# Kernel optimization log

Hardware: AMD Instinct MI355X
Metric: run time of the kernel (lower is better)

Reference implementation:

```python
import jax, jax.numpy as jnp
import numpy as np

N, IN_DIM, HID, OUT_DIM = 1024, 128, 128, 128


def setup_inputs() -> dict:
    key = jax.random.key(0)
    ks = jax.random.split(key, 7)
    s_in = 1.0 / np.sqrt(IN_DIM)
    s_h = 1.0 / np.sqrt(HID)
    return {
        "x": jax.random.normal(ks[0], (N, IN_DIM), jnp.float32),
        "W1": jax.random.normal(ks[1], (IN_DIM, HID), jnp.float32) * s_in,
        "b1": jax.random.normal(ks[2], (HID,), jnp.float32) * s_in,
        "W2": jax.random.normal(ks[3], (HID, 1), jnp.float32) * s_h,
        "b2": jax.random.normal(ks[4], (1,), jnp.float32) * s_h,
        "Wg": jax.random.normal(ks[5], (IN_DIM, OUT_DIM), jnp.float32) * s_in,
        "bg": jax.random.normal(ks[6], (OUT_DIM,), jnp.float32) * s_in,
    }


def reference(x, W1, b1, W2, b2, Wg, bg):
    # Pairwise abs-diff: [N, N, in_dim]
    diff = jnp.abs(x[:, None, :] - x[None, :, :])
    # 2-layer MLP -> scalar edge logit, then sigmoid -> dense adjacency [N, N]
    h = jax.nn.relu(jnp.einsum("ijd,dh->ijh", diff, W1) + b1)
    adj = jax.nn.sigmoid(jnp.einsum("ijh,ho->ijo", h, W2)[..., 0] + b2[0])
    # sigmoid > 0 everywhere => dense_to_sparse keeps ALL N^2 edges incl. diagonal;
    # PyG gcn_norm then adds no extra self-loops. Symmetric GCN normalization:
    deg = adj.sum(axis=1)  # adj is symmetric (|x_i - x_j| symmetric)
    dinv = jax.lax.rsqrt(deg)
    a_norm = dinv[:, None] * adj * dinv[None, :]
    out = a_norm @ (x @ Wg) + bg
    out = jnp.where(out > 0, out, 0.2 * out)  # leaky_relu(0.2)
    return out, adj
```

## Files before the change

kernel.cpp:

```cpp
#include <hip/hip_runtime.h>
#include <hip/hip_bf16.h>
#include <math.h>

typedef __attribute__((ext_vector_type(8))) _Float16 half8;
typedef __attribute__((ext_vector_type(2))) _Float16 half2v;
typedef __attribute__((ext_vector_type(4))) float f32x4;
typedef __attribute__((ext_vector_type(4))) unsigned int u32x4;

#define NPT 1024
#define D   128

__device__ __forceinline__ unsigned int absdiff_pk(unsigned int a, unsigned int b) {
  half2v d = __builtin_bit_cast(half2v, a) - __builtin_bit_cast(half2v, b);
  return __builtin_bit_cast(unsigned int, d) & 0x7FFF7FFFu;
}
__device__ __forceinline__ unsigned int pk_max(unsigned int a, unsigned int b) {
  unsigned int r;
  asm("v_pk_max_f16 %0, %1, %2" : "=v"(r) : "v"(a), "v"(b));
  return r;
}
__device__ __forceinline__ unsigned int pkrtz(float lo, float hi) {
  return __builtin_bit_cast(unsigned int, __builtin_amdgcn_cvt_pkrtz(lo, hi));
}
__device__ __forceinline__ float fdot2(unsigned int a, unsigned int b, float c) {
  return __builtin_amdgcn_fdot2(__builtin_bit_cast(half2v, a),
                                __builtin_bit_cast(half2v, b), c, false);
}

__global__ __launch_bounds__(128) void k_prep(const float* __restrict__ x,
                                              const float* __restrict__ W1,
                                              const float* __restrict__ Wg,
                                              float* __restrict__ deg,
                                              unsigned short* __restrict__ xsw,
                                              unsigned short* __restrict__ w1p,
                                              unsigned short* __restrict__ xwghT) {
  __shared__ float xi[D];
  const int i = blockIdx.x;
  const int t = threadIdx.x;
  const float xv = x[i * D + t];
  xi[t] = xv;
  if (t == 0) deg[i] = 0.f;
  const _Float16 hv = (_Float16)xv;
  const int byte = i * 256 + ((2 * t) ^ ((i & 7) << 4));
  *(unsigned short*)((unsigned char*)xsw + byte) =
      __builtin_bit_cast(unsigned short, hv);
  if (i < 128) {
    const _Float16 wv = (_Float16)W1[t * 128 + i];
    w1p[((t >> 3) * 128 + i) * 8 + (t & 7)] = __builtin_bit_cast(unsigned short, wv);
  }
  __syncthreads();
  float a0 = 0.f, a1 = 0.f, a2 = 0.f, a3 = 0.f;
#pragma unroll 8
  for (int k = 0; k < D; k += 4) {
    a0 += xi[k + 0] * Wg[(k + 0) * D + t];
    a1 += xi[k + 1] * Wg[(k + 1) * D + t];
    a2 += xi[k + 2] * Wg[(k + 2) * D + t];
    a3 += xi[k + 3] * Wg[(k + 3) * D + t];
  }
  const _Float16 av = (_Float16)((a0 + a1) + (a2 + a3));
  xwghT[t * NPT + i] = __builtin_bit_cast(unsigned short, av);
}

__global__ __launch_bounds__(256, 2) void k_adj(const unsigned short* __restrict__ xsw,
                                                const unsigned short* __restrict__ w1p,
                                                const float* __restrict__ b1,
                                                const float* __restrict__ W2,
                                                const float* __restrict__ b2,
                                                float* __restrict__ adj) {
  __shared__ float sbuf[4][17 * 68];
  const int tid  = threadIdx.x;
  const int lane = tid & 63;
  const int w    = tid >> 6;
  const int l15  = lane & 15;
  const int g    = lane >> 4;
  const int i   = blockIdx.x * 4 + w;
  const int c   = blockIdx.y;
  const int i2  = 1023 - i;
  const int a   = i >> 4;
  const int n_i = 64 - a;
  const int ustart = c * 16;
  const int uend   = (c == 3) ? 65 : (ustart + 16);
  const int len    = uend - ustart;
  const int nvals  = len * 16;
  const int asc    = (blockIdx.y >> 1) & 1;

  half8 w1f[4][8];
#pragma unroll
  for (int ks = 0; ks < 4; ++ks)
#pragma unroll
    for (int ht = 0; ht < 8; ++ht)
      w1f[ks][ht] = *(const half8*)(w1p + ((ks * 4 + g) * 128 + ht * 16 + l15) * 8);

  unsigned int nb1pk[8][2], w2pk[8][2];
  float c0 = 0.f;
#pragma unroll
  for (int ht = 0; ht < 8; ++ht) {
    const f32x4 bv = *(const f32x4*)&b1[ht * 16 + g * 4];
    const f32x4 wv = *(const f32x4*)&W2[ht * 16 + g * 4];
    c0 += bv[0] * wv[0] + bv[1] * wv[1] + bv[2] * wv[2] + bv[3] * wv[3];
    nb1pk[ht][0] = pkrtz(-bv[0], -bv[1]);
    nb1pk[ht][1] = pkrtz(-bv[2], -bv[3]);
    w2pk[ht][0] = pkrtz(wv[0], wv[1]);
    w2pk[ht][1] = pkrtz(wv[2], wv[3]);
  }
  c0 += __shfl_xor(c0, 16);
  c0 += __shfl_xor(c0, 32);
  const float B2 = b2[0] + c0;

  const unsigned char* xsb = (const unsigned char*)xsw;
  const unsigned char* jlane = xsb + l15 * 256;
  const int sxJ = (l15 & 7) << 4;
  const int kb0 = (0 * 64 + g * 16) ^ sxJ;
  const int kb1 = (1 * 64 + g * 16) ^ sxJ;
  const int kb2 = (2 * 64 + g * 16) ^ sxJ;
  const int kb3 = (3 * 64 + g * 16) ^ sxJ;

  float* sbw = sbuf[w];
  u32x4 xiu[4];
  int row_cur = -1;

  u32x4 jr0, jr1, jr2, jr3;
  {
    const int u0 = asc ? ustart : (uend - 1);
    const int grp0 = (u0 < n_i) ? (a + u0) : (u0 - 1);
    const unsigned char* cur = jlane + grp0 * 4096;
    jr0 = *(const u32x4*)(cur + kb0);
    jr1 = *(const u32x4*)(cur + kb1);
    jr2 = *(const u32x4*)(cur + kb2);
    jr3 = *(const u32x4*)(cur + kb3);
  }

#pragma unroll 1
  for (int t = 0; t < len; ++t) {
    const int u = asc ? (ustart + t) : (uend - 1 - t);
    const int row = (u < n_i) ? i : i2;
    if (row != row_cur) {
      row_cur = row;
      const unsigned char* xrow = xsb + row * 256;
      const int sxI = (row & 7) << 4;
#pragma unroll
      for (int ks = 0; ks < 4; ++ks)
        xiu[ks] = *(const u32x4*)(xrow + ((ks * 64 + g * 16) ^ sxI));
    }
    const int tn = (t + 1 < len) ? (t + 1) : t;
    const int un = asc ? (ustart + tn) : (uend - 1 - tn);
    const int grpn = (un < n_i) ? (a + un) : (un - 1);
    const unsigned char* nrow = jlane + grpn * 4096;

    f32x4 acc[8];
#pragma unroll
    for (int ht = 0; ht < 8; ++ht) acc[ht] = f32x4{0.f, 0.f, 0.f, 0.f};

    __builtin_amdgcn_s_setprio(1);
    {
      u32x4 afu;
#pragma unroll
      for (int p4 = 0; p4 < 4; ++p4) afu[p4] = absdiff_pk(jr0[p4], xiu[0][p4]);
      jr0 = *(const u32x4*)(nrow + kb0);
      const half8 af = __builtin_bit_cast(half8, afu);
#pragma unroll
      for (int ht = 0; ht < 8; ++ht)
        acc[ht] = __builtin_amdgcn_mfma_f32_16x16x32_f16(w1f[0][ht], af, acc[ht], 0, 0, 0);
    }
    {
      u32x4 afu;
#pragma unroll
      for (int p4 = 0; p4 < 4; ++p4) afu[p4] = absdiff_pk(jr1[p4], xiu[1][p4]);
      jr1 = *(const u32x4*)(nrow + kb1);
      const half8 af = __builtin_bit_cast(half8, afu);
#pragma unroll
      for (int ht = 0; ht < 8; ++ht)
        acc[ht] = __builtin_amdgcn_mfma_f32_16x16x32_f16(w1f[1][ht], af, acc[ht], 0, 0, 0);
    }
    {
      u32x4 afu;
#pragma unroll
      for (int p4 = 0; p4 < 4; ++p4) afu[p4] = absdiff_pk(jr2[p4], xiu[2][p4]);
      jr2 = *(const u32x4*)(nrow + kb2);
      const half8 af = __builtin_bit_cast(half8, afu);
#pragma unroll
      for (int ht = 0; ht < 8; ++ht)
        acc[ht] = __builtin_amdgcn_mfma_f32_16x16x32_f16(w1f[2][ht], af, acc[ht], 0, 0, 0);
    }
    {
      u32x4 afu;
#pragma unroll
      for (int p4 = 0; p4 < 4; ++p4) afu[p4] = absdiff_pk(jr3[p4], xiu[3][p4]);
      jr3 = *(const u32x4*)(nrow + kb3);
      const half8 af = __builtin_bit_cast(half8, afu);
#pragma unroll
      for (int ht = 0; ht < 8; ++ht)
        acc[ht] = __builtin_amdgcn_mfma_f32_16x16x32_f16(w1f[3][ht], af, acc[ht], 0, 0, 0);
    }
    __builtin_amdgcn_s_setprio(0);

    float sA = 0.f, sB = 0.f, sC = 0.f, sD = 0.f;
#pragma unroll
    for (int ht = 0; ht < 8; ht += 2) {
      unsigned int h0a = pk_max(pkrtz(acc[ht][0], acc[ht][1]), nb1pk[ht][0]);
      unsigned int h0b = pk_max(pkrtz(acc[ht][2], acc[ht][3]), nb1pk[ht][1]);
      unsigned int h1a = pk_max(pkrtz(acc[ht + 1][0], acc[ht + 1][1]), nb1pk[ht + 1][0]);
      unsigned int h1b = pk_max(pkrtz(acc[ht + 1][2], acc[ht + 1][3]), nb1pk[ht + 1][1]);
      sA = fdot2(h0a, w2pk[ht][0], sA);
      sB = fdot2(h0b, w2pk[ht][1], sB);
      sC = fdot2(h1a, w2pk[ht + 1][0], sC);
      sD = fdot2(h1b, w2pk[ht + 1][1], sD);
    }
    sbw[t * 68 + lane] = (sA + sB) + (sC + sD);
  }

#pragma unroll 1
  for (int it = 0; it < 5; ++it) {
    const int p = it * 64 + lane;
    if (p < nvals) {
      const int tt = p >> 4;
      const int j = p & 15;
      const int u = asc ? (ustart + tt) : (uend - 1 - tt);
      const int row = (u < n_i) ? i : i2;
      const int grp = (u < n_i) ? (a + u) : (u - 1);
      const float s = sbw[tt * 68 + j] + sbw[tt * 68 + 16 + j] +
                      sbw[tt * 68 + 32 + j] + sbw[tt * 68 + 48 + j];
      const float sig = 1.f / (1.f + __expf(-(s + B2)));
      adj[row * NPT + grp * 16 + j] = sig;
    }
  }
}

__global__ __launch_bounds__(256) void k_symdeg(float* __restrict__ adj,
                                                float* __restrict__ deg) {
  __shared__ float lds[4][16][17];
  const int tid  = threadIdx.x;
  const int lane = tid & 63;
  const int w    = tid >> 6;
  const int r16 = lane & 15;
  const int c4  = (lane >> 4) * 4;

  if (blockIdx.x < 504) {
    const int t = blockIdx.x * 4 + w;
    int R = (int)((1.0f + sqrtf(1.0f + 8.0f * (float)t)) * 0.5f);
    if (R * (R - 1) / 2 > t) --R;
    if ((R + 1) * R / 2 <= t) ++R;
    const int C = t - R * (R - 1) / 2;

    const f32x4 v = *(const f32x4*)&adj[(C * 16 + r16) * NPT + R * 16 + c4];
    float rs = (v[0] + v[1]) + (v[2] + v[3]);
    rs += __shfl_xor(rs, 16);
    rs += __shfl_xor(rs, 32);
    if (lane < 16) atomicAdd(&deg[C * 16 + r16], rs);
#pragma unroll
    for (int e = 0; e < 4; ++e) lds[w][c4 + e][r16] = v[e];
    f32x4 o;
#pragma unroll
    for (int e = 0; e < 4; ++e) o[e] = lds[w][r16][c4 + e];
    *(f32x4*)&adj[(R * 16 + r16) * NPT + C * 16 + c4] = o;
    float cs = (o[0] + o[1]) + (o[2] + o[3]);
    cs += __shfl_xor(cs, 16);
    cs += __shfl_xor(cs, 32);
    if (lane < 16) atomicAdd(&deg[R * 16 + r16], cs);
  } else {
    const int T = (blockIdx.x - 504) * 4 + w;
    const f32x4 v = *(const f32x4*)&adj[(T * 16 + r16) * NPT + T * 16 + c4];
    float rs = (v[0] + v[1]) + (v[2] + v[3]);
    rs += __shfl_xor(rs, 16);
    rs += __shfl_xor(rs, 32);
    if (lane < 16) atomicAdd(&deg[T * 16 + r16], rs);
  }
}

__global__ __launch_bounds__(128) void k_d1(const float* __restrict__ adj,
                                            const unsigned short* __restrict__ xwghT,
                                            const float* __restrict__ deg,
                                            const float* __restrict__ bg,
                                            float* __restrict__ outp) {
  __shared__ unsigned short dvh[NPT];
  const int tid  = threadIdx.x;
  const int lane = tid & 63;
  const int w    = tid >> 6;
  const int l15  = lane & 15;
  const int g    = lane >> 4;
  const int i0 = blockIdx.x * 16;
  const int t0 = (blockIdx.y * 2 + w) * 16;

#pragma unroll
  for (int it = 0; it < 8; ++it) {
    const int idx = it * 128 + tid;
    const _Float16 dh = (_Float16)rsqrtf(deg[idx]);
    dvh[idx] = __builtin_bit_cast(unsigned short, dh);
  }
  __syncthreads();

  f32x4 acc{0.f, 0.f, 0.f, 0.f};
#pragma unroll 2
  for (int ch = 0; ch < 32; ++ch) {
    const int kofs = ch * 32 + g * 8;
    const half8 af = *(const half8*)(xwghT + (t0 + l15) * NPT + kofs);
    const f32x4 av0 = *(const f32x4*)&adj[(i0 + l15) * NPT + kofs];
    const f32x4 av1 = *(const f32x4*)&adj[(i0 + l15) * NPT + kofs + 4];
    const half2v* dq = (const half2v*)(dvh + kofs);
    u32x4 bu;
    bu[0] = __builtin_bit_cast(unsigned int,
        half2v(__builtin_bit_cast(half2v, pkrtz(av0[0], av0[1])) * dq[0]));
    bu[1] = __builtin_bit_cast(unsigned int,
        half2v(__builtin_bit_cast(half2v, pkrtz(av0[2], av0[3])) * dq[1]));
    bu[2] = __builtin_bit_cast(unsigned int,
        half2v(__builtin_bit_cast(half2v, pkrtz(av1[0], av1[1])) * dq[2]));
    bu[3] = __builtin_bit_cast(unsigned int,
        half2v(__builtin_bit_cast(half2v, pkrtz(av1[2], av1[3])) * dq[3]));
    acc = __builtin_amdgcn_mfma_f32_16x16x32_f16(__builtin_bit_cast(half8, af),
                                                 __builtin_bit_cast(half8, bu), acc, 0, 0, 0);
  }
  const float di = rsqrtf(deg[i0 + l15]);
  const f32x4 bgv = *(const f32x4*)&bg[t0 + g * 4];
  f32x4 o;
#pragma unroll
  for (int r = 0; r < 4; ++r) {
    const float v = acc[r] * di + bgv[r];
    o[r] = v > 0.f ? v : 0.2f * v;
  }
  *(f32x4*)&outp[(i0 + l15) * D + t0 + g * 4] = o;
}

extern "C" void kernel_launch(void* const* d_in, const int* in_sizes, int n_in,
                              void* d_out, int out_size, void* d_ws, size_t ws_size,
                              hipStream_t stream) {
  const float* x  = (const float*)d_in[0];
  const float* W1 = (const float*)d_in[1];
  const float* b1 = (const float*)d_in[2];
  const float* W2 = (const float*)d_in[3];
  const float* b2 = (const float*)d_in[4];
  const float* Wg = (const float*)d_in[5];
  const float* bg = (const float*)d_in[6];

  float* outp = (float*)d_out;
  float* adj  = outp + NPT * D;
  unsigned char* ws = (unsigned char*)d_ws;
  float* deg            = (float*)ws;
  unsigned short* xsw   = (unsigned short*)(ws + 4096);
  unsigned short* w1p   = (unsigned short*)(ws + 4096 + 262144);
  unsigned short* xwghT = (unsigned short*)(ws + 4096 + 262144 + 32768);

  k_prep<<<NPT, 128, 0, stream>>>(x, W1, Wg, deg, xsw, w1p, xwghT);
  k_adj<<<dim3(128, 4), 256, 0, stream>>>(xsw, w1p, b1, W2, b2, adj);
  k_symdeg<<<520, 256, 0, stream>>>(adj, deg);
  k_d1<<<dim3(64, 4), 128, 0, stream>>>(adj, xwghT, deg, bg, outp);
}
```

Baseline: 44.08 us.

## Split hidden dimension across wave pairs in k_adj and widen k_d1 blocks

k_adj now assigns each row to a pair of waves that each compute half of the 128 hidden units, halving per-wave W1 fragment registers and accumulators. This raises occupancy (launch bounds 3) and doubles the grid, at the cost of an added block barrier and an LDS reduction over eight partials. k_d1 now processes all 128 output columns per block using 4 waves with two MFMA tiles each. The adj tile and degree scaling are then converted once per block rather than four times across blocks, though the grid shrinks to 64 blocks.

New measurement: 53.62 us. +21.6%, slower.

```diff
diff --git a/kernel.cpp b/kernel.cpp
--- a/kernel.cpp
+++ b/kernel.cpp
@@ -61,19 +61,21 @@
   xwghT[t * NPT + i] = __builtin_bit_cast(unsigned short, av);
 }
 
-__global__ __launch_bounds__(256, 2) void k_adj(const unsigned short* __restrict__ xsw,
+__global__ __launch_bounds__(256, 3) void k_adj(const unsigned short* __restrict__ xsw,
                                                 const unsigned short* __restrict__ w1p,
                                                 const float* __restrict__ b1,
                                                 const float* __restrict__ W2,
                                                 const float* __restrict__ b2,
                                                 float* __restrict__ adj) {
-  __shared__ float sbuf[4][17 * 68];
+  __shared__ float sbuf[2][17 * 136];
   const int tid  = threadIdx.x;
   const int lane = tid & 63;
   const int w    = tid >> 6;
   const int l15  = lane & 15;
   const int g    = lane >> 4;
-  const int i   = blockIdx.x * 4 + w;
+  const int hh   = w & 1;
+  const int pair = w >> 1;
+  const int i   = blockIdx.x * 2 + pair;
   const int c   = blockIdx.y;
   const int i2  = 1023 - i;
   const int a   = i >> 4;
@@ -82,26 +84,32 @@
   const int uend   = (c == 3) ? 65 : (ustart + 16);
   const int len    = uend - ustart;
   const int nvals  = len * 16;
-  const int asc    = (blockIdx.y >> 1) & 1;
-
-  half8 w1f[4][8];
+  const int asc    = (blockIdx.x ^ (blockIdx.y >> 1)) & 1;
+
+  half8 w1f[4][4];
 #pragma unroll
   for (int ks = 0; ks < 4; ++ks)
 #pragma unroll
-    for (int ht = 0; ht < 8; ++ht)
-      w1f[ks][ht] = *(const half8*)(w1p + ((ks * 4 + g) * 128 + ht * 16 + l15) * 8);
-
-  unsigned int nb1pk[8][2], w2pk[8][2];
+    for (int ht2 = 0; ht2 < 4; ++ht2)
+      w1f[ks][ht2] = *(const half8*)(w1p +
+          ((ks * 4 + g) * 128 + hh * 64 + ht2 * 16 + l15) * 8);
+
+  unsigned int nb1pk[4][2], w2pk[4][2];
   float c0 = 0.f;
 #pragma unroll
   for (int ht = 0; ht < 8; ++ht) {
     const f32x4 bv = *(const f32x4*)&b1[ht * 16 + g * 4];
     const f32x4 wv = *(const f32x4*)&W2[ht * 16 + g * 4];
     c0 += bv[0] * wv[0] + bv[1] * wv[1] + bv[2] * wv[2] + bv[3] * wv[3];
-    nb1pk[ht][0] = pkrtz(-bv[0], -bv[1]);
-    nb1pk[ht][1] = pkrtz(-bv[2], -bv[3]);
-    w2pk[ht][0] = pkrtz(wv[0], wv[1]);
-    w2pk[ht][1] = pkrtz(wv[2], wv[3]);
+  }
+#pragma unroll
+  for (int ht2 = 0; ht2 < 4; ++ht2) {
+    const f32x4 bv = *(const f32x4*)&b1[hh * 64 + ht2 * 16 + g * 4];
+    const f32x4 wv = *(const f32x4*)&W2[hh * 64 + ht2 * 16 + g * 4];
+    nb1pk[ht2][0] = pkrtz(-bv[0], -bv[1]);
+    nb1pk[ht2][1] = pkrtz(-bv[2], -bv[3]);
+    w2pk[ht2][0] = pkrtz(wv[0], wv[1]);
+    w2pk[ht2][1] = pkrtz(wv[2], wv[3]);
   }
   c0 += __shfl_xor(c0, 16);
   c0 += __shfl_xor(c0, 32);
@@ -115,7 +123,7 @@
   const int kb2 = (2 * 64 + g * 16) ^ sxJ;
   const int kb3 = (3 * 64 + g * 16) ^ sxJ;
 
-  float* sbw = sbuf[w];
+  float* sbw = sbuf[pair];
   u32x4 xiu[4];
   int row_cur = -1;
 
@@ -147,9 +155,9 @@
     const int grpn = (un < n_i) ? (a + un) : (un - 1);
     const unsigned char* nrow = jlane + grpn * 4096;
 
-    f32x4 acc[8];
-#pragma unroll
-    for (int ht = 0; ht < 8; ++ht) acc[ht] = f32x4{0.f, 0.f, 0.f, 0.f};
+    f32x4 acc[4];
+#pragma unroll
+    for (int ht2 = 0; ht2 < 4; ++ht2) acc[ht2] = f32x4{0.f, 0.f, 0.f, 0.f};
 
     __builtin_amdgcn_s_setprio(1);
     {
@@ -159,8 +167,8 @@
       jr0 = *(const u32x4*)(nrow + kb0);
       const half8 af = __builtin_bit_cast(half8, afu);
 #pragma unroll
-      for (int ht = 0; ht < 8; ++ht)
-        acc[ht] = __builtin_amdgcn_mfma_f32_16x16x32_f16(w1f[0][ht], af, acc[ht], 0, 0, 0);
+      for (int ht2 = 0; ht2 < 4; ++ht2)
+        acc[ht2] = __builtin_amdgcn_mfma_f32_16x16x32_f16(w1f[0][ht2], af, acc[ht2], 0, 0, 0);
     }
     {
       u32x4 afu;
@@ -169,8 +177,8 @@
       jr1 = *(const u32x4*)(nrow + kb1);
       const half8 af = __builtin_bit_cast(half8, afu);
 #pragma unroll
-      for (int ht = 0; ht < 8; ++ht)
-        acc[ht] = __builtin_amdgcn_mfma_f32_16x16x32_f16(w1f[1][ht], af, acc[ht], 0, 0, 0);
+      for (int ht2 = 0; ht2 < 4; ++ht2)
+        acc[ht2] = __builtin_amdgcn_mfma_f32_16x16x32_f16(w1f[1][ht2], af, acc[ht2], 0, 0, 0);
     }
     {
       u32x4 afu;
@@ -179,8 +187,8 @@
       jr2 = *(const u32x4*)(nrow + kb2);
       const half8 af = __builtin_bit_cast(half8, afu);
 #pragma unroll
-      for (int ht = 0; ht < 8; ++ht)
-        acc[ht] = __builtin_amdgcn_mfma_f32_16x16x32_f16(w1f[2][ht], af, acc[ht], 0, 0, 0);
+      for (int ht2 = 0; ht2 < 4; ++ht2)
+        acc[ht2] = __builtin_amdgcn_mfma_f32_16x16x32_f16(w1f[2][ht2], af, acc[ht2], 0, 0, 0);
     }
     {
       u32x4 afu;
@@ -189,37 +197,41 @@
       jr3 = *(const u32x4*)(nrow + kb3);
       const half8 af = __builtin_bit_cast(half8, afu);
 #pragma unroll
-      for (int ht = 0; ht < 8; ++ht)
-        acc[ht] = __builtin_amdgcn_mfma_f32_16x16x32_f16(w1f[3][ht], af, acc[ht], 0, 0, 0);
+      for (int ht2 = 0; ht2 < 4; ++ht2)
+        acc[ht2] = __builtin_amdgcn_mfma_f32_16x16x32_f16(w1f[3][ht2], af, acc[ht2], 0, 0, 0);
     }
     __builtin_amdgcn_s_setprio(0);
 
     float sA = 0.f, sB = 0.f, sC = 0.f, sD = 0.f;
 #pragma unroll
-    for (int ht = 0; ht < 8; ht += 2) {
-      unsigned int h0a = pk_max(pkrtz(acc[ht][0], acc[ht][1]), nb1pk[ht][0]);
-      unsigned int h0b = pk_max(pkrtz(acc[ht][2], acc[ht][3]), nb1pk[ht][1]);
-      unsigned int h1a = pk_max(pkrtz(acc[ht + 1][0], acc[ht + 1][1]), nb1pk[ht + 1][0]);
-      unsigned int h1b = pk_max(pkrtz(acc[ht + 1][2], acc[ht + 1][3]), nb1pk[ht + 1][1]);
-      sA = fdot2(h0a, w2pk[ht][0], sA);
-      sB = fdot2(h0b, w2pk[ht][1], sB);
-      sC = fdot2(h1a, w2pk[ht + 1][0], sC);
-      sD = fdot2(h1b, w2pk[ht + 1][1], sD);
-    }
-    sbw[t * 68 + lane] = (sA + sB) + (sC + sD);
-  }
-
+    for (int ht2 = 0; ht2 < 4; ht2 += 2) {
+      unsigned int h0a = pk_max(pkrtz(acc[ht2][0], acc[ht2][1]), nb1pk[ht2][0]);
+      unsigned int h0b = pk_max(pkrtz(acc[ht2][2], acc[ht2][3]), nb1pk[ht2][1]);
+      unsigned int h1a = pk_max(pkrtz(acc[ht2 + 1][0], acc[ht2 + 1][1]), nb1pk[ht2 + 1][0]);
+      unsigned int h1b = pk_max(pkrtz(acc[ht2 + 1][2], acc[ht2 + 1][3]), nb1pk[ht2 + 1][1]);
+      sA = fdot2(h0a, w2pk[ht2][0], sA);
+      sB = fdot2(h0b, w2pk[ht2][1], sB);
+      sC = fdot2(h1a, w2pk[ht2 + 1][0], sC);
+      sD = fdot2(h1b, w2pk[ht2 + 1][1], sD);
+    }
+    sbw[t * 136 + hh * 64 + lane] = (sA + sB) + (sC + sD);
+  }
+
+  __syncthreads();
+
+  const int q = tid & 127;
 #pragma unroll 1
-  for (int it = 0; it < 5; ++it) {
-    const int p = it * 64 + lane;
+  for (int it = 0; it < 3; ++it) {
+    const int p = it * 128 + q;
     if (p < nvals) {
       const int tt = p >> 4;
       const int j = p & 15;
       const int u = asc ? (ustart + tt) : (uend - 1 - tt);
       const int row = (u < n_i) ? i : i2;
       const int grp = (u < n_i) ? (a + u) : (u - 1);
-      const float s = sbw[tt * 68 + j] + sbw[tt * 68 + 16 + j] +
-                      sbw[tt * 68 + 32 + j] + sbw[tt * 68 + 48 + j];
+      const float* sp = &sbw[tt * 136 + j];
+      const float s = ((sp[0] + sp[16]) + (sp[32] + sp[48])) +
+                      ((sp[64] + sp[80]) + (sp[96] + sp[112]));
       const float sig = 1.f / (1.f + __expf(-(s + B2)));
       adj[row * NPT + grp * 16 + j] = sig;
     }
@@ -267,7 +279,7 @@
   }
 }
 
-__global__ __launch_bounds__(128) void k_d1(const float* __restrict__ adj,
+__global__ __launch_bounds__(256) void k_d1(const float* __restrict__ adj,
                                             const unsigned short* __restrict__ xwghT,
                                             const float* __restrict__ deg,
                                             const float* __restrict__ bg,
@@ -279,21 +291,19 @@
   const int l15  = lane & 15;
   const int g    = lane >> 4;
   const int i0 = blockIdx.x * 16;
-  const int t0 = (blockIdx.y * 2 + w) * 16;
-
-#pragma unroll
-  for (int it = 0; it < 8; ++it) {
-    const int idx = it * 128 + tid;
+
+#pragma unroll
+  for (int it = 0; it < 4; ++it) {
+    const int idx = it * 256 + tid;
     const _Float16 dh = (_Float16)rsqrtf(deg[idx]);
     dvh[idx] = __builtin_bit_cast(unsigned short, dh);
   }
   __syncthreads();
 
-  f32x4 acc{0.f, 0.f, 0.f, 0.f};
+  f32x4 acc[2] = {f32x4{0.f, 0.f, 0.f, 0.f}, f32x4{0.f, 0.f, 0.f, 0.f}};
 #pragma unroll 2
   for (int ch = 0; ch < 32; ++ch) {
     const int kofs = ch * 32 + g * 8;
-    const half8 af = *(const half8*)(xwghT + (t0 + l15) * NPT + kofs);
     const f32x4 av0 = *(const f32x4*)&adj[(i0 + l15) * NPT + kofs];
     const f32x4 av1 = *(const f32x4*)&adj[(i0 + l15) * NPT + kofs + 4];
     const half2v* dq = (const half2v*)(dvh + kofs);
@@ -306,18 +316,27 @@
         half2v(__builtin_bit_cast(half2v, pkrtz(av1[0], av1[1])) * dq[2]));
     bu[3] = __builtin_bit_cast(unsigned int,
         half2v(__builtin_bit_cast(half2v, pkrtz(av1[2], av1[3])) * dq[3]));
-    acc = __builtin_amdgcn_mfma_f32_16x16x32_f16(__builtin_bit_cast(half8, af),
-                                                 __builtin_bit_cast(half8, bu), acc, 0, 0, 0);
+    const half8 bf = __builtin_bit_cast(half8, bu);
+#pragma unroll
+    for (int tt = 0; tt < 2; ++tt) {
+      const int trow = w * 32 + tt * 16 + l15;
+      const half8 af = *(const half8*)(xwghT + trow * NPT + kofs);
+      acc[tt] = __builtin_amdgcn_mfma_f32_16x16x32_f16(af, bf, acc[tt], 0, 0, 0);
+    }
   }
   const float di = rsqrtf(deg[i0 + l15]);
-  const f32x4 bgv = *(const f32x4*)&bg[t0 + g * 4];
-  f32x4 o;
-#pragma unroll
-  for (int r = 0; r < 4; ++r) {
-    const float v = acc[r] * di + bgv[r];
-    o[r] = v > 0.f ? v : 0.2f * v;
-  }
-  *(f32x4*)&outp[(i0 + l15) * D + t0 + g * 4] = o;
+#pragma unroll
+  for (int tt = 0; tt < 2; ++tt) {
+    const int t0 = w * 32 + tt * 16;
+    const f32x4 bgv = *(const f32x4*)&bg[t0 + g * 4];
+    f32x4 o;
+#pragma unroll
+    for (int r = 0; r < 4; ++r) {
+      const float v = acc[tt][r] * di + bgv[r];
+      o[r] = v > 0.f ? v : 0.2f * v;
+    }
+    *(f32x4*)&outp[(i0 + l15) * D + t0 + g * 4] = o;
+  }
 }
 
 extern "C" void kernel_launch(void* const* d_in, const int* in_sizes, int n_in,
@@ -340,7 +359,7 @@
   unsigned short* xwghT = (unsigned short*)(ws + 4096 + 262144 + 32768);
 
   k_prep<<<NPT, 128, 0, stream>>>(x, W1, Wg, deg, xsw, w1p, xwghT);
-  k_adj<<<dim3(128, 4), 256, 0, stream>>>(xsw, w1p, b1, W2, b2, adj);
+  k_adj<<<dim3(256, 4), 256, 0, stream>>>(xsw, w1p, b1, W2, b2, adj);
   k_symdeg<<<520, 256, 0, stream>>>(adj, deg);
-  k_d1<<<dim3(64, 4), 128, 0, stream>>>(adj, xwghT, deg, bg, outp);
-}
+  k_d1<<<64, 256, 0, stream>>>(adj, xwghT, deg, bg, outp);
+}
```
